# Performance work log

Hardware: AMD Instinct MI355X
Metric: run time of the kernel (lower is better)

The kernel has to match this reference:

```python
import jax, jax.numpy as jnp
import numpy as np

B, S, E, H, L = 4, 512, 768, 12, 12
D = E // H
FF = 4 * E
EPS = 1e-5
SCALE = jnp.float32(768.0 ** 0.5)  # emb_size ** (1/2), applied AFTER softmax per source


def setup_inputs() -> dict:
    key = jax.random.key(0)
    ks = jax.random.split(key, 18)
    std = 0.02
    n = lambda k, shp: (jax.random.normal(k, shp, jnp.float32) * std)
    return {
        "x": jax.random.normal(ks[0], (B, S, E), jnp.float32),
        "Wqkv": n(ks[1], (L, E, 3 * E)),
        "bqkv": n(ks[2], (L, 3 * E)),
        "Wp": n(ks[3], (L, E, E)),
        "bp": n(ks[4], (L, E)),
        "W1": n(ks[5], (L, E, FF)),
        "b1": n(ks[6], (L, FF)),
        "W2": n(ks[7], (L, FF, E)),
        "b2": n(ks[8], (L, E)),
        "ln1_g": jnp.ones((L, E), jnp.float32), "ln1_b": jnp.zeros((L, E), jnp.float32),
        "ln2_g": jnp.ones((L, E), jnp.float32), "ln2_b": jnp.zeros((L, E), jnp.float32),
        "ln3_g": jnp.ones((L, E), jnp.float32), "ln3_b": jnp.zeros((L, E), jnp.float32),
        "ln4_g": jnp.ones((L, E), jnp.float32), "ln4_b": jnp.zeros((L, E), jnp.float32),
    }


def _ln(x, g, b):
    m = jnp.mean(x, axis=-1, keepdims=True)
    v = jnp.mean(jnp.square(x - m), axis=-1, keepdims=True)
    return (x - m) * jax.lax.rsqrt(v + EPS) * g + b


def _block(x, p):
    Wqkv, bqkv, Wp, bp, W1, b1, W2, b2, g1, be1, g2, be2, g3, be3, g4, be4 = p
    # --- attention branch ---
    h = _ln(x, g1, be1)
    qkv = h @ Wqkv + bqkv                      # [B,S,3E]
    qkv = qkv.reshape(B, S, H, D, 3)           # qkv is innermost factor in source rearrange
    q = jnp.transpose(qkv[..., 0], (0, 2, 1, 3))  # [B,H,S,D]
    k = jnp.transpose(qkv[..., 1], (0, 2, 1, 3))
    v = jnp.transpose(qkv[..., 2], (0, 2, 1, 3))
    energy = jnp.einsum('bhqd,bhkd->bhqk', q, k)
    att = jax.nn.softmax(energy, axis=-1) / SCALE  # NOTE: scaling AFTER softmax (faithful)
    o = jnp.einsum('bhqk,bhkd->bhqd', att, v)
    o = jnp.transpose(o, (0, 2, 1, 3)).reshape(B, S, E)
    o = o @ Wp + bp
    r1 = _ln(o, g2, be2) + x                   # first ResidualAdd (final LN inside branch)
    # --- feed-forward branch ---
    f = _ln(r1, g3, be3)
    f = jax.nn.gelu(f @ W1 + b1, approximate=False)
    f = f @ W2 + b2
    r2 = _ln(f, g4, be4) + r1                  # second ResidualAdd
    return x + r2                              # outer residual: x = x + block(x)


def reference(x, Wqkv, bqkv, Wp, bp, W1, b1, W2, b2,
              ln1_g, ln1_b, ln2_g, ln2_b, ln3_g, ln3_b, ln4_g, ln4_b):
    params = (Wqkv, bqkv, Wp, bp, W1, b1, W2, b2,
              ln1_g, ln1_b, ln2_g, ln2_b, ln3_g, ln3_b, ln4_g, ln4_b)
    out, _ = jax.lax.scan(lambda c, p: (_block(c, p), None), x, params)
    return out
```

## Files before the change

### kernel.cpp

```cpp
#include <hip/hip_runtime.h>
#include <hip/hip_bf16.h>
#include <stdint.h>

#define LAYERS 12
#define M_ROWS 2048
#define E_DIM 768
#define FF_DIM 3072
#define QKV_DIM 2304
#define SCALE_INV 0.036084391824351615f

typedef __hip_bfloat16 bf16;
typedef __attribute__((ext_vector_type(8))) __bf16 bf16x8;
typedef __attribute__((ext_vector_type(4))) float f32x4;

__device__ __forceinline__ float bf2f(bf16 v) { return __bfloat162float(v); }
__device__ __forceinline__ bf16 f2bf(float v) { return __float2bfloat16(v); }

__device__ __forceinline__ float gelu_f(float x) {
  return 0.5f * x * (1.0f + erff(x * 0.70710678118654752f));
}

__global__ __launch_bounds__(256) void transpose_k(
    const float* __restrict__ w0, const float* __restrict__ w1,
    const float* __restrict__ w2, const float* __restrict__ w3,
    bf16* __restrict__ t0, bf16* __restrict__ t1,
    bf16* __restrict__ t2, bf16* __restrict__ t3)
{
  __shared__ float T[32][33];
  int bid = blockIdx.x;
  const float* src; bf16* dst; int K, N, tile;
  if (bid < 1728)      { src = w0; dst = t0; K = 768;  N = 2304; tile = bid; }
  else if (bid < 2304) { src = w1; dst = t1; K = 768;  N = 768;  tile = bid - 1728; }
  else if (bid < 4608) { src = w2; dst = t2; K = 768;  N = 3072; tile = bid - 2304; }
  else                 { src = w3; dst = t3; K = 3072; N = 768;  tile = bid - 4608; }
  int tilesN = N >> 5;
  int tk = tile / tilesN;
  int tn = tile - tk * tilesN;
  int tx = threadIdx.x & 31, ty = threadIdx.x >> 5;
  int k0 = tk << 5, n0 = tn << 5;
#pragma unroll
  for (int i = 0; i < 4; i++)
    T[ty + i * 8][tx] = src[(size_t)(k0 + ty + i * 8) * N + n0 + tx];
  __syncthreads();
#pragma unroll
  for (int i = 0; i < 4; i++)
    dst[(size_t)(n0 + ty + i * 8) * K + k0 + tx] = f2bf(T[tx][ty + i * 8]);
}

template<int OUT_BF16, int NADD>
__global__ __launch_bounds__(256) void ln_k(
    const float* in, const float* gamma, const float* beta,
    const float* add0, const float* add1, void* outp)
{
  int row = blockIdx.x, tid = threadIdx.x;
  const float* x = in + (size_t)row * 768;
  float v[3]; float s = 0.f, sq = 0.f;
#pragma unroll
  for (int j = 0; j < 3; j++) {
    v[j] = x[tid + j * 256];
    s += v[j]; sq += v[j] * v[j];
  }
#pragma unroll
  for (int off = 32; off; off >>= 1) {
    s += __shfl_xor(s, off);
    sq += __shfl_xor(sq, off);
  }
  __shared__ float red[8];
  int wv = tid >> 6;
  if ((tid & 63) == 0) { red[wv] = s; red[4 + wv] = sq; }
  __syncthreads();
  s  = red[0] + red[1] + red[2] + red[3];
  sq = red[4] + red[5] + red[6] + red[7];
  float mean = s * (1.0f / 768.0f);
  float var  = sq * (1.0f / 768.0f) - mean * mean;
  float rstd = rsqrtf(var + 1e-5f);
#pragma unroll
  for (int j = 0; j < 3; j++) {
    int c = tid + j * 256;
    float val = (v[j] - mean) * rstd * gamma[c] + beta[c];
    if (NADD >= 1) val += add0[(size_t)row * 768 + c];
    if (NADD >= 2) val += add1[(size_t)row * 768 + c];
    if (OUT_BF16) ((bf16*)outp)[(size_t)row * 768 + c] = f2bf(val);
    else          ((float*)outp)[(size_t)row * 768 + c] = val;
  }
}

template<int OUT_MODE>
__global__ __launch_bounds__(256) void gemm_k(
    const bf16* __restrict__ A, const bf16* __restrict__ BT,
    const float* __restrict__ bias, void* __restrict__ Cout,
    bf16* __restrict__ qo, bf16* __restrict__ ko, bf16* __restrict__ vo,
    int N, int K)
{
  __shared__ __align__(16) bf16 Als[64 * 32];
  __shared__ __align__(16) bf16 Bls[64 * 32];
  int tid = threadIdx.x;
  int lane = tid & 63, wave = tid >> 6;
  int wm = (wave >> 1) * 32, wn = (wave & 1) * 32;
  int m0 = (blockIdx.x & 31) << 6;
  int n0 = (blockIdx.x >> 5) << 6;
  const bf16* Ap = A + (size_t)m0 * K;
  const bf16* Bp = BT + (size_t)n0 * K;
  int sr = tid >> 2;
  int sc = (tid & 3) * 8;
  f32x4 acc[2][2] = {};
  for (int k0 = 0; k0 < K; k0 += 32) {
    uint4 av = *(const uint4*)(Ap + (size_t)sr * K + k0 + sc);
    uint4 bv = *(const uint4*)(Bp + (size_t)sr * K + k0 + sc);
    __syncthreads();
    *(uint4*)&Als[tid * 8] = av;
    *(uint4*)&Bls[tid * 8] = bv;
    __syncthreads();
    int ko8 = (lane >> 4) * 8;
    bf16x8 af[2], bfr[2];
#pragma unroll
    for (int i = 0; i < 2; i++)
      af[i] = *(const bf16x8*)&Als[(wm + i * 16 + (lane & 15)) * 32 + ko8];
#pragma unroll
    for (int j = 0; j < 2; j++)
      bfr[j] = *(const bf16x8*)&Bls[(wn + j * 16 + (lane & 15)) * 32 + ko8];
#pragma unroll
    for (int i = 0; i < 2; i++)
#pragma unroll
      for (int j = 0; j < 2; j++)
        acc[i][j] = __builtin_amdgcn_mfma_f32_16x16x32_bf16(af[i], bfr[j], acc[i][j], 0, 0, 0);
  }
#pragma unroll
  for (int i = 0; i < 2; i++) {
    int mbase = m0 + wm + i * 16 + ((lane >> 4) << 2);
#pragma unroll
    for (int j = 0; j < 2; j++) {
      int n = n0 + wn + j * 16 + (lane & 15);
      float bvs = bias[n];
      if (OUT_MODE == 3) {
        int h = n / 192;
        int rm = n - h * 192;
        int d = rm / 3;
        int t = rm - d * 3;
#pragma unroll
        for (int rg = 0; rg < 4; rg++) {
          int m = mbase + rg;
          float val = acc[i][j][rg] + bvs;
          int b = m >> 9, sIdx = m & 511;
          int bh = b * 12 + h;
          if (t == 2)
            vo[(size_t)((bh << 6) + d) * 512 + sIdx] = f2bf(val);
          else {
            bf16* dsts = (t == 0) ? qo : ko;
            dsts[(size_t)((bh << 9) + sIdx) * 64 + d] = f2bf(val);
          }
        }
      } else {
#pragma unroll
        for (int rg = 0; rg < 4; rg++) {
          int m = mbase + rg;
          float val = acc[i][j][rg] + bvs;
          if (OUT_MODE == 0)      ((float*)Cout)[(size_t)m * N + n] = val;
          else if (OUT_MODE == 1) ((bf16*)Cout)[(size_t)m * N + n] = f2bf(val);
          else                    ((bf16*)Cout)[(size_t)m * N + n] = f2bf(gelu_f(val));
        }
      }
    }
  }
}

#define PSTR 80
__global__ __launch_bounds__(256) void attn_k(
    const bf16* __restrict__ q, const bf16* __restrict__ k,
    const bf16* __restrict__ vT, bf16* __restrict__ o)
{
  __shared__ __align__(16) bf16 Kls[64 * 64];
  __shared__ __align__(16) bf16 Vls[64 * 64];
  __shared__ __align__(16) bf16 Pls[4][16 * PSTR];
  int tid = threadIdx.x;
  int lane = tid & 63, w = tid >> 6;
  int l15 = lane & 15, l4 = lane >> 4;
  int qt = blockIdx.x & 7;
  int bh = blockIdx.x >> 3;
  size_t base = (size_t)bh * 32768;

  const bf16* qrowp = q + base + (size_t)(qt * 64 + w * 16 + l15) * 64 + l4 * 8;
  bf16x8 qf0 = *(const bf16x8*)qrowp;
  bf16x8 qf1 = *(const bf16x8*)(qrowp + 32);

  float mrow[4] = {-1e30f, -1e30f, -1e30f, -1e30f};
  float lsum[4] = {0.f, 0.f, 0.f, 0.f};
  f32x4 Oacc[4] = {};
  const f32x4 zed = {0.f, 0.f, 0.f, 0.f};
  bf16* pw = &Pls[w][0];

  for (int kt = 0; kt < 8; kt++) {
    __syncthreads();
#pragma unroll
    for (int rep = 0; rep < 2; rep++) {
      int c = tid + rep * 256;
      int row = c >> 3, col8 = (c & 7) * 8;
      *(uint4*)&Kls[row * 64 + col8] =
          *(const uint4*)(k + base + (size_t)(kt * 64 + row) * 64 + col8);
      *(uint4*)&Vls[row * 64 + col8] =
          *(const uint4*)(vT + base + (size_t)row * 512 + kt * 64 + col8);
    }
    __syncthreads();
    f32x4 e[4];
#pragma unroll
    for (int jt = 0; jt < 4; jt++) {
      bf16x8 kf0 = *(const bf16x8*)&Kls[(jt * 16 + l15) * 64 + l4 * 8];
      bf16x8 kf1 = *(const bf16x8*)&Kls[(jt * 16 + l15) * 64 + l4 * 8 + 32];
      e[jt] = __builtin_amdgcn_mfma_f32_16x16x32_bf16(qf0, kf0, zed, 0, 0, 0);
      e[jt] = __builtin_amdgcn_mfma_f32_16x16x32_bf16(qf1, kf1, e[jt], 0, 0, 0);
    }
    float al[4];
#pragma unroll
    for (int rg = 0; rg < 4; rg++) {
      float mn = fmaxf(fmaxf(e[0][rg], e[1][rg]), fmaxf(e[2][rg], e[3][rg]));
#pragma unroll
      for (int off = 1; off < 16; off <<= 1) mn = fmaxf(mn, __shfl_xor(mn, off));
      float mnew = fmaxf(mrow[rg], mn);
      al[rg] = __expf(mrow[rg] - mnew);
      mrow[rg] = mnew;
    }
    float rs[4] = {0.f, 0.f, 0.f, 0.f};
#pragma unroll
    for (int jt = 0; jt < 4; jt++)
#pragma unroll
      for (int rg = 0; rg < 4; rg++) {
        float p = __expf(e[jt][rg] - mrow[rg]);
        rs[rg] += p;
        pw[(l4 * 4 + rg) * PSTR + jt * 16 + l15] = f2bf(p);
      }
#pragma unroll
    for (int rg = 0; rg < 4; rg++) {
#pragma unroll
      for (int off = 1; off < 16; off <<= 1) rs[rg] += __shfl_xor(rs[rg], off);
      lsum[rg] = lsum[rg] * al[rg] + rs[rg];
    }
#pragma unroll
    for (int dt = 0; dt < 4; dt++)
#pragma unroll
      for (int rg = 0; rg < 4; rg++) Oacc[dt][rg] *= al[rg];
    bf16x8 pf0 = *(const bf16x8*)&pw[l15 * PSTR + l4 * 8];
    bf16x8 pf1 = *(const bf16x8*)&pw[l15 * PSTR + l4 * 8 + 32];
#pragma unroll
    for (int dt = 0; dt < 4; dt++) {
      bf16x8 vf0 = *(const bf16x8*)&Vls[(dt * 16 + l15) * 64 + l4 * 8];
      bf16x8 vf1 = *(const bf16x8*)&Vls[(dt * 16 + l15) * 64 + l4 * 8 + 32];
      Oacc[dt] = __builtin_amdgcn_mfma_f32_16x16x32_bf16(pf0, vf0, Oacc[dt], 0, 0, 0);
      Oacc[dt] = __builtin_amdgcn_mfma_f32_16x16x32_bf16(pf1, vf1, Oacc[dt], 0, 0, 0);
    }
  }
  int b = bh / 12, h = bh - b * 12;
#pragma unroll
  for (int rg = 0; rg < 4; rg++) {
    int qrow = qt * 64 + w * 16 + l4 * 4 + rg;
    float inv = SCALE_INV / lsum[rg];
    size_t rowoff = (size_t)(b * 512 + qrow) * 768 + h * 64;
#pragma unroll
    for (int dt = 0; dt < 4; dt++)
      o[rowoff + dt * 16 + l15] = f2bf(Oacc[dt][rg] * inv);
  }
}

extern "C" void kernel_launch(void* const* d_in, const int* in_sizes, int n_in,
                              void* d_out, int out_size, void* d_ws, size_t ws_size,
                              hipStream_t stream)
{
  const float* x    = (const float*)d_in[0];
  const float* Wqkv = (const float*)d_in[1];
  const float* bqkv = (const float*)d_in[2];
  const float* Wp   = (const float*)d_in[3];
  const float* bp   = (const float*)d_in[4];
  const float* W1   = (const float*)d_in[5];
  const float* b1   = (const float*)d_in[6];
  const float* W2   = (const float*)d_in[7];
  const float* b2   = (const float*)d_in[8];
  const float* g1  = (const float*)d_in[9];
  const float* be1 = (const float*)d_in[10];
  const float* g2  = (const float*)d_in[11];
  const float* be2 = (const float*)d_in[12];
  const float* g3  = (const float*)d_in[13];
  const float* be3 = (const float*)d_in[14];
  const float* g4  = (const float*)d_in[15];
  const float* be4 = (const float*)d_in[16];
  float* xout = (float*)d_out;

  char* ws = (char*)d_ws;
  size_t off = 0;
  auto alloc = [&](size_t bytes) -> char* {
    char* p = ws + off;
    off += (bytes + 255) & ~(size_t)255;
    return p;
  };
  const size_t NTOK = (size_t)M_ROWS * E_DIM;
  bf16*  qb  = (bf16*)alloc(NTOK * 2);
  bf16*  kb  = (bf16*)alloc(NTOK * 2);
  bf16*  vb  = (bf16*)alloc(NTOK * 2);
  bf16*  hb  = (bf16*)alloc(NTOK * 2);
  bf16*  ob  = (bf16*)alloc(NTOK * 2);
  bf16*  f1b = (bf16*)alloc((size_t)M_ROWS * FF_DIM * 2);
  float* tmp = (float*)alloc(NTOK * 4);
  float* r1  = (float*)alloc(NTOK * 4);
  bf16*  tq  = (bf16*)alloc((size_t)768 * 2304 * 2);
  bf16*  tp  = (bf16*)alloc((size_t)768 * 768 * 2);
  bf16*  t1  = (bf16*)alloc((size_t)768 * 3072 * 2);
  bf16*  t2  = (bf16*)alloc((size_t)3072 * 768 * 2);
  if (off > ws_size) {
    hipMemsetAsync(d_out, 0x7f, (size_t)out_size * 4, stream);
    return;
  }

  hipMemcpyAsync(d_out, x, (size_t)out_size * 4, hipMemcpyDeviceToDevice, stream);

  for (int l = 0; l < LAYERS; l++) {
    const float* wq  = Wqkv + (size_t)l * 768 * 2304;
    const float* wp_ = Wp   + (size_t)l * 768 * 768;
    const float* w1_ = W1   + (size_t)l * 768 * 3072;
    const float* w2_ = W2   + (size_t)l * 3072 * 768;

    transpose_k<<<6912, 256, 0, stream>>>(wq, wp_, w1_, w2_, tq, tp, t1, t2);

    ln_k<1, 0><<<2048, 256, 0, stream>>>(xout, g1 + l * 768, be1 + l * 768,
                                         nullptr, nullptr, hb);
    gemm_k<3><<<32 * 36, 256, 0, stream>>>(hb, tq, bqkv + (size_t)l * 2304,
                                           nullptr, qb, kb, vb, 2304, 768);
    attn_k<<<384, 256, 0, stream>>>(qb, kb, vb, ob);
    gemm_k<0><<<32 * 12, 256, 0, stream>>>(ob, tp, bp + (size_t)l * 768,
                                           tmp, nullptr, nullptr, nullptr, 768, 768);
    ln_k<0, 1><<<2048, 256, 0, stream>>>(tmp, g2 + l * 768, be2 + l * 768,
                                         xout, nullptr, r1);
    ln_k<1, 0><<<2048, 256, 0, stream>>>(r1, g3 + l * 768, be3 + l * 768,
                                         nullptr, nullptr, hb);
    gemm_k<2><<<32 * 48, 256, 0, stream>>>(hb, t1, b1 + (size_t)l * 3072,
                                           f1b, nullptr, nullptr, nullptr, 3072, 768);
    gemm_k<0><<<32 * 12, 256, 0, stream>>>(f1b, t2, b2 + (size_t)l * 768,
                                           tmp, nullptr, nullptr, nullptr, 768, 3072);
    ln_k<0, 2><<<2048, 256, 0, stream>>>(tmp, g4 + l * 768, be4 + l * 768,
                                         r1, xout, xout);
  }
}
```

Measured before the change: 2.145 ms.

## Double-buffer GEMM with async global-to-LDS loads, larger tiles, split-K for N=768

```diff
diff --git a/kernel.cpp b/kernel.cpp
--- a/kernel.cpp
+++ b/kernel.cpp
@@ -18,6 +18,12 @@
 
 __device__ __forceinline__ float gelu_f(float x) {
   return 0.5f * x * (1.0f + erff(x * 0.70710678118654752f));
+}
+
+__device__ __forceinline__ void async16(const bf16* g, bf16* l) {
+  __builtin_amdgcn_global_load_lds(
+      (const __attribute__((address_space(1))) void*)g,
+      (__attribute__((address_space(3))) void*)l, 16, 0, 0);
 }
 
 __global__ __launch_bounds__(256) void transpose_k(
@@ -47,18 +53,22 @@
     dst[(size_t)(n0 + ty + i * 8) * K + k0 + tx] = f2bf(T[tx][ty + i * 8]);
 }
 
-template<int OUT_BF16, int NADD>
+template<int OUT_BF16, int NADD, int NPART>
 __global__ __launch_bounds__(256) void ln_k(
-    const float* in, const float* gamma, const float* beta,
-    const float* add0, const float* add1, void* outp)
+    const float* __restrict__ in, const float* __restrict__ gamma,
+    const float* __restrict__ beta, const float* __restrict__ add0,
+    const float* __restrict__ add1, void* __restrict__ outp)
 {
   int row = blockIdx.x, tid = threadIdx.x;
-  const float* x = in + (size_t)row * 768;
+  size_t rb = (size_t)row * 768;
   float v[3]; float s = 0.f, sq = 0.f;
 #pragma unroll
   for (int j = 0; j < 3; j++) {
-    v[j] = x[tid + j * 256];
-    s += v[j]; sq += v[j] * v[j];
+    int c = tid + j * 256;
+    float x = in[rb + c];
+    if (NPART == 2) x += in[(size_t)M_ROWS * 768 + rb + c];
+    v[j] = x;
+    s += x; sq += x * x;
   }
 #pragma unroll
   for (int off = 32; off; off >>= 1) {
@@ -78,60 +88,74 @@
   for (int j = 0; j < 3; j++) {
     int c = tid + j * 256;
     float val = (v[j] - mean) * rstd * gamma[c] + beta[c];
-    if (NADD >= 1) val += add0[(size_t)row * 768 + c];
-    if (NADD >= 2) val += add1[(size_t)row * 768 + c];
-    if (OUT_BF16) ((bf16*)outp)[(size_t)row * 768 + c] = f2bf(val);
-    else          ((float*)outp)[(size_t)row * 768 + c] = val;
-  }
-}
-
-template<int OUT_MODE>
-__global__ __launch_bounds__(256) void gemm_k(
+    if (NADD >= 1) val += add0[rb + c];
+    if (NADD >= 2) val += add1[rb + c];
+    if (OUT_BF16) ((bf16*)outp)[rb + c] = f2bf(val);
+    else          ((float*)outp)[rb + c] = val;
+  }
+}
+
+template<int OUT_MODE, int NSPLIT>
+__global__ __launch_bounds__(256) void gemm2_k(
     const bf16* __restrict__ A, const bf16* __restrict__ BT,
     const float* __restrict__ bias, void* __restrict__ Cout,
     bf16* __restrict__ qo, bf16* __restrict__ ko, bf16* __restrict__ vo,
     int N, int K)
 {
-  __shared__ __align__(16) bf16 Als[64 * 32];
-  __shared__ __align__(16) bf16 Bls[64 * 32];
+  __shared__ __align__(16) bf16 Als[2][128 * 32];
+  __shared__ __align__(16) bf16 Bls[2][64 * 32];
   int tid = threadIdx.x;
-  int lane = tid & 63, wave = tid >> 6;
-  int wm = (wave >> 1) * 32, wn = (wave & 1) * 32;
-  int m0 = (blockIdx.x & 31) << 6;
-  int n0 = (blockIdx.x >> 5) << 6;
+  int lane = tid & 63, w = tid >> 6;
+  int l15 = lane & 15, l4 = lane >> 4;
+  int Nt = N >> 6;
+  int mt = blockIdx.x / Nt, ntile = blockIdx.x - mt * Nt;
+  int m0 = mt << 7, n0 = ntile << 6;
+  int sp = (NSPLIT > 1) ? blockIdx.y : 0;
+  int Kc = K / NSPLIT;
+  int kbeg = sp * Kc, kend = kbeg + Kc;
   const bf16* Ap = A + (size_t)m0 * K;
   const bf16* Bp = BT + (size_t)n0 * K;
-  int sr = tid >> 2;
-  int sc = (tid & 3) * 8;
-  f32x4 acc[2][2] = {};
-  for (int k0 = 0; k0 < K; k0 += 32) {
-    uint4 av = *(const uint4*)(Ap + (size_t)sr * K + k0 + sc);
-    uint4 bv = *(const uint4*)(Bp + (size_t)sr * K + k0 + sc);
+  int ar = tid >> 2;
+  int ac = (tid & 3) * 8;
+
+  f32x4 acc[2][4] = {};
+
+  async16(Ap + (size_t)ar * K + kbeg + ac,        &Als[0][w * 512]);
+  async16(Ap + (size_t)(ar + 64) * K + kbeg + ac, &Als[0][2048 + w * 512]);
+  async16(Bp + (size_t)ar * K + kbeg + ac,        &Bls[0][w * 512]);
+  __syncthreads();
+
+  int cur = 0;
+  for (int k0 = kbeg; k0 < kend; k0 += 32) {
+    if (k0 + 32 < kend) {
+      int kn = k0 + 32;
+      async16(Ap + (size_t)ar * K + kn + ac,        &Als[cur ^ 1][w * 512]);
+      async16(Ap + (size_t)(ar + 64) * K + kn + ac, &Als[cur ^ 1][2048 + w * 512]);
+      async16(Bp + (size_t)ar * K + kn + ac,        &Bls[cur ^ 1][w * 512]);
+    }
+    bf16x8 af[2], bfr[4];
+#pragma unroll
+    for (int i = 0; i < 2; i++)
+      af[i] = *(const bf16x8*)&Als[cur][(w * 32 + i * 16 + l15) * 32 + l4 * 8];
+#pragma unroll
+    for (int j = 0; j < 4; j++)
+      bfr[j] = *(const bf16x8*)&Bls[cur][(j * 16 + l15) * 32 + l4 * 8];
+#pragma unroll
+    for (int i = 0; i < 2; i++)
+#pragma unroll
+      for (int j = 0; j < 4; j++)
+        acc[i][j] = __builtin_amdgcn_mfma_f32_16x16x32_bf16(af[i], bfr[j], acc[i][j], 0, 0, 0);
     __syncthreads();
-    *(uint4*)&Als[tid * 8] = av;
-    *(uint4*)&Bls[tid * 8] = bv;
-    __syncthreads();
-    int ko8 = (lane >> 4) * 8;
-    bf16x8 af[2], bfr[2];
-#pragma unroll
-    for (int i = 0; i < 2; i++)
-      af[i] = *(const bf16x8*)&Als[(wm + i * 16 + (lane & 15)) * 32 + ko8];
-#pragma unroll
-    for (int j = 0; j < 2; j++)
-      bfr[j] = *(const bf16x8*)&Bls[(wn + j * 16 + (lane & 15)) * 32 + ko8];
-#pragma unroll
-    for (int i = 0; i < 2; i++)
-#pragma unroll
-      for (int j = 0; j < 2; j++)
-        acc[i][j] = __builtin_amdgcn_mfma_f32_16x16x32_bf16(af[i], bfr[j], acc[i][j], 0, 0, 0);
-  }
+    cur ^= 1;
+  }
+
 #pragma unroll
   for (int i = 0; i < 2; i++) {
-    int mbase = m0 + wm + i * 16 + ((lane >> 4) << 2);
-#pragma unroll
-    for (int j = 0; j < 2; j++) {
-      int n = n0 + wn + j * 16 + (lane & 15);
-      float bvs = bias[n];
+    int mbase = m0 + w * 32 + i * 16 + (l4 << 2);
+#pragma unroll
+    for (int j = 0; j < 4; j++) {
+      int n = n0 + j * 16 + l15;
+      float bvs = (NSPLIT == 1 || sp == 0) ? bias[n] : 0.0f;
       if (OUT_MODE == 3) {
         int h = n / 192;
         int rm = n - h * 192;
@@ -155,9 +179,12 @@
         for (int rg = 0; rg < 4; rg++) {
           int m = mbase + rg;
           float val = acc[i][j][rg] + bvs;
-          if (OUT_MODE == 0)      ((float*)Cout)[(size_t)m * N + n] = val;
-          else if (OUT_MODE == 1) ((bf16*)Cout)[(size_t)m * N + n] = f2bf(val);
-          else                    ((bf16*)Cout)[(size_t)m * N + n] = f2bf(gelu_f(val));
+          if (OUT_MODE == 0)
+            ((float*)Cout)[(size_t)sp * M_ROWS * N + (size_t)m * N + n] = val;
+          else if (OUT_MODE == 1)
+            ((bf16*)Cout)[(size_t)m * N + n] = f2bf(val);
+          else
+            ((bf16*)Cout)[(size_t)m * N + n] = f2bf(gelu_f(val));
         }
       }
     }
@@ -297,7 +324,7 @@
   bf16*  hb  = (bf16*)alloc(NTOK * 2);
   bf16*  ob  = (bf16*)alloc(NTOK * 2);
   bf16*  f1b = (bf16*)alloc((size_t)M_ROWS * FF_DIM * 2);
-  float* tmp = (float*)alloc(NTOK * 4);
+  float* tmp = (float*)alloc(NTOK * 4 * 2);
   float* r1  = (float*)alloc(NTOK * 4);
   bf16*  tq  = (bf16*)alloc((size_t)768 * 2304 * 2);
   bf16*  tp  = (bf16*)alloc((size_t)768 * 768 * 2);
@@ -318,22 +345,22 @@
 
     transpose_k<<<6912, 256, 0, stream>>>(wq, wp_, w1_, w2_, tq, tp, t1, t2);
 
-    ln_k<1, 0><<<2048, 256, 0, stream>>>(xout, g1 + l * 768, be1 + l * 768,
-                                         nullptr, nullptr, hb);
-    gemm_k<3><<<32 * 36, 256, 0, stream>>>(hb, tq, bqkv + (size_t)l * 2304,
-                                           nullptr, qb, kb, vb, 2304, 768);
+    ln_k<1, 0, 1><<<2048, 256, 0, stream>>>(xout, g1 + l * 768, be1 + l * 768,
+                                            nullptr, nullptr, hb);
+    gemm2_k<3, 1><<<dim3(16 * 36, 1), 256, 0, stream>>>(
+        hb, tq, bqkv + (size_t)l * 2304, nullptr, qb, kb, vb, 2304, 768);
     attn_k<<<384, 256, 0, stream>>>(qb, kb, vb, ob);
-    gemm_k<0><<<32 * 12, 256, 0, stream>>>(ob, tp, bp + (size_t)l * 768,
-                                           tmp, nullptr, nullptr, nullptr, 768, 768);
-    ln_k<0, 1><<<2048, 256, 0, stream>>>(tmp, g2 + l * 768, be2 + l * 768,
-                                         xout, nullptr, r1);
-    ln_k<1, 0><<<2048, 256, 0, stream>>>(r1, g3 + l * 768, be3 + l * 768,
-                                         nullptr, nullptr, hb);
-    gemm_k<2><<<32 * 48, 256, 0, stream>>>(hb, t1, b1 + (size_t)l * 3072,
-                                           f1b, nullptr, nullptr, nullptr, 3072, 768);
-    gemm_k<0><<<32 * 12, 256, 0, stream>>>(f1b, t2, b2 + (size_t)l * 768,
-                                           tmp, nullptr, nullptr, nullptr, 768, 3072);
-    ln_k<0, 2><<<2048, 256, 0, stream>>>(tmp, g4 + l * 768, be4 + l * 768,
-                                         r1, xout, xout);
-  }
-}
+    gemm2_k<0, 2><<<dim3(16 * 12, 2), 256, 0, stream>>>(
+        ob, tp, bp + (size_t)l * 768, tmp, nullptr, nullptr, nullptr, 768, 768);
+    ln_k<0, 1, 2><<<2048, 256, 0, stream>>>(tmp, g2 + l * 768, be2 + l * 768,
+                                            xout, nullptr, r1);
+    ln_k<1, 0, 1><<<2048, 256, 0, stream>>>(r1, g3 + l * 768, be3 + l * 768,
+                                            nullptr, nullptr, hb);
+    gemm2_k<2, 1><<<dim3(16 * 48, 1), 256, 0, stream>>>(
+        hb, t1, b1 + (size_t)l * 3072, f1b, nullptr, nullptr, nullptr, 3072, 768);
+    gemm2_k<0, 2><<<dim3(16 * 12, 2), 256, 0, stream>>>(
+        f1b, t2, b2 + (size_t)l * 768, tmp, nullptr, nullptr, nullptr, 768, 3072);
+    ln_k<0, 2, 2><<<2048, 256, 0, stream>>>(tmp, g4 + l * 768, be4 + l * 768,
+                                            r1, xout, xout);
+  }
+}
```

Result: faster. 1.984 ms (-7.5%).
